# Kernel tuning notes

Hardware: AMD Instinct MI355X
Metric: run time of the kernel (lower is better)

## Reference

```python
import jax, jax.numpy as jnp
import numpy as np

N_QUBITS = 6
DIM = 2 ** N_QUBITS  # 64


def _b(t, nd):
    # broadcast a (B,) per-sample angle factor (or scalar) against a state slice of rank nd
    if jnp.ndim(t) == 0:
        return t
    return t.reshape((t.shape[0],) + (1,) * (nd - 1))


def _ry(state, theta, q):
    ax = q + 1
    s0 = jnp.take(state, 0, axis=ax)
    s1 = jnp.take(state, 1, axis=ax)
    h = theta * 0.5
    c = _b(jnp.cos(h), s0.ndim)
    s = _b(jnp.sin(h), s0.ndim)
    return jnp.stack([c * s0 - s * s1, s * s0 + c * s1], axis=ax)


def _rx(state, theta, q):
    ax = q + 1
    s0 = jnp.take(state, 0, axis=ax)
    s1 = jnp.take(state, 1, axis=ax)
    h = theta * 0.5
    c = _b(jnp.cos(h), s0.ndim)
    s = _b(jnp.sin(h), s0.ndim)
    return jnp.stack([c * s0 - 1j * s * s1, -1j * s * s0 + c * s1], axis=ax)


def _rz(state, theta, q):
    ax = q + 1
    s0 = jnp.take(state, 0, axis=ax)
    s1 = jnp.take(state, 1, axis=ax)
    h = theta * 0.5
    p0 = _b(jnp.exp(-1j * h), s0.ndim)
    p1 = _b(jnp.exp(1j * h), s0.ndim)
    return jnp.stack([p0 * s0, p1 * s1], axis=ax)


def _cnot(state, ctrl, tgt):
    ca = ctrl + 1
    s0 = jnp.take(state, 0, axis=ca)
    s1 = jnp.take(state, 1, axis=ca)
    ta = tgt + 1 if tgt < ctrl else tgt  # target axis after removing control axis
    s1 = jnp.flip(s1, axis=ta)
    return jnp.stack([s0, s1], axis=ca)


def quantum_circuit(inputs, weights):
    # inputs: (B, 6) float; weights: (5, 6) float -> (B, 6) PauliZ expectations
    B = inputs.shape[0]
    scaled = jnp.clip(inputs, -1.0, 1.0) * jnp.pi
    state = jnp.zeros((B,) + (2,) * N_QUBITS, dtype=jnp.complex64)
    state = state.at[(slice(None),) + (0,) * N_QUBITS].set(1.0)
    for i in range(N_QUBITS):
        state = _ry(state, scaled[:, i], i)
    for i in range(N_QUBITS):
        state = _rx(state, weights[0, i], i)
        state = _rz(state, weights[1, i], i)
    for i in range(N_QUBITS - 1):
        state = _cnot(state, i, i + 1)
    state = _cnot(state, N_QUBITS - 1, 0)
    for i in range(N_QUBITS):
        state = _ry(state, weights[2, i], i)
        state = _rz(state, weights[3, i], i)
    for i in range(0, N_QUBITS, 2):
        state = _cnot(state, i, (i + 1) % N_QUBITS)
    for i in range(N_QUBITS):
        state = _rx(state, weights[4, i], i)
    probs = (state.real ** 2 + state.imag ** 2).reshape(B, DIM)
    # Z eigenvalue table: qubit q is bit (5-q) of the flat index
    k = jnp.arange(DIM)
    z = (1 - 2 * ((k[None, :] >> (N_QUBITS - 1 - jnp.arange(N_QUBITS)[:, None])) & 1)).astype(jnp.float32)
    return probs @ z.T  # (B, 6)


def setup_inputs() -> dict:
    key = jax.random.key(0)
    ks = jax.random.split(key, 13)
    B, n_symptoms, n_dep, nq = 262144, 128, 20, N_QUBITS

    def lin(k, fi, fo):
        bound = 1.0 / np.sqrt(fi)
        kw, kb = jax.random.split(k)
        W = jax.random.uniform(kw, (fi, fo), jnp.float32, -bound, bound)
        b = jax.random.uniform(kb, (fo,), jnp.float32, -bound, bound)
        return W, b

    x = jax.random.normal(ks[0], (B, n_symptoms), jnp.float32)
    W1, b1 = lin(ks[1], n_symptoms, 32)
    W2, b2 = lin(ks[2], 32, 16)
    W3, b3 = lin(ks[3], 16, nq)
    qw = jax.random.normal(ks[4], (5, nq), jnp.float32)
    W4, b4 = lin(ks[5], nq, 16)
    W5, b5 = lin(ks[6], 16, n_dep)
    return {"x": x, "W1": W1, "b1": b1, "W2": W2, "b2": b2, "W3": W3, "b3": b3,
            "qw": qw, "W4": W4, "b4": b4, "W5": W5, "b5": b5}


def reference(x, W1, b1, W2, b2, W3, b3, qw, W4, b4, W5, b5):
    h = jax.nn.relu(x @ W1 + b1)            # Dropout(0.2) is identity at eval
    h = jax.nn.relu(h @ W2 + b2)
    pre = jnp.tanh(h @ W3 + b3)             # (B, 6)
    # Original detaches before the quantum circuit -> stop_gradient for fidelity
    q_out = quantum_circuit(jax.lax.stop_gradient(pre), jax.lax.stop_gradient(qw))
    h = jax.nn.relu(q_out @ W4 + b4)
    return h @ W5 + b5                      # (B, n_departments)
```

## Files before the change

kernel.cpp:

```cpp
#include <hip/hip_runtime.h>
#include <hip/hip_bf16.h>
#include <math.h>

#define PI_F 3.14159265358979323846f

typedef float f32x4 __attribute__((ext_vector_type(4)));
typedef short bf16x8 __attribute__((ext_vector_type(8)));

__device__ __forceinline__ unsigned short bf_hi(float f) {
    return (unsigned short)(__float_as_uint(f) >> 16);
}
__device__ __forceinline__ float from_bf(unsigned short h) {
    return __uint_as_float(((unsigned)h) << 16);
}

__global__ __launch_bounds__(64) void build_u(const float* __restrict__ qw,
                                              float* __restrict__ Umat) {
    const int l = threadIdx.x;
    const int b = blockIdx.x;

    float ar = (l == b) ? 1.0f : 0.0f;
    float ai = 0.0f;

    #pragma unroll
    for (int i = 0; i < 6; ++i) {
        const int mask = 1 << (5 - i);
        float th = 0.5f * qw[0 * 6 + i];
        float c = cosf(th), sn = sinf(th);
        float pr = __shfl_xor(ar, mask);
        float pi = __shfl_xor(ai, mask);
        float nr = c * ar + sn * pi;
        float ni = c * ai - sn * pr;
        ar = nr; ai = ni;
        th = 0.5f * qw[1 * 6 + i];
        c = cosf(th); sn = sinf(th);
        float zn = (l & mask) ? 1.0f : -1.0f;
        nr = c * ar - zn * sn * ai;
        ni = c * ai + zn * sn * ar;
        ar = nr; ai = ni;
    }

    #pragma unroll
    for (int i = 0; i < 6; ++i) {
        const int ctrl = i, tgt = (i + 1) % 6;
        const int cm = 1 << (5 - ctrl), tm = 1 << (5 - tgt);
        float pr = __shfl_xor(ar, tm);
        float pi = __shfl_xor(ai, tm);
        bool take = (l & cm) != 0;
        ar = take ? pr : ar;
        ai = take ? pi : ai;
    }

    #pragma unroll
    for (int i = 0; i < 6; ++i) {
        const int mask = 1 << (5 - i);
        float th = 0.5f * qw[2 * 6 + i];
        float c = cosf(th), sn = sinf(th);
        float pr = __shfl_xor(ar, mask);
        float pi = __shfl_xor(ai, mask);
        float sg = (l & mask) ? sn : -sn;
        float nr = c * ar + sg * pr;
        float ni = c * ai + sg * pi;
        ar = nr; ai = ni;
        th = 0.5f * qw[3 * 6 + i];
        c = cosf(th); sn = sinf(th);
        float zn = (l & mask) ? 1.0f : -1.0f;
        nr = c * ar - zn * sn * ai;
        ni = c * ai + zn * sn * ar;
        ar = nr; ai = ni;
    }

    #pragma unroll
    for (int i = 0; i < 6; i += 2) {
        const int cm = 1 << (5 - i), tm = 1 << (5 - (i + 1));
        float pr = __shfl_xor(ar, tm);
        float pi = __shfl_xor(ai, tm);
        bool take = (l & cm) != 0;
        ar = take ? pr : ar;
        ai = take ? pi : ai;
    }

    #pragma unroll
    for (int i = 0; i < 6; ++i) {
        const int mask = 1 << (5 - i);
        float th = 0.5f * qw[4 * 6 + i];
        float c = cosf(th), sn = sinf(th);
        float pr = __shfl_xor(ar, mask);
        float pi = __shfl_xor(ai, mask);
        float nr = c * ar + sn * pi;
        float ni = c * ai - sn * pr;
        ar = nr; ai = ni;
    }

    Umat[(l * 64 + b) * 2 + 0] = ar;
    Umat[(l * 64 + b) * 2 + 1] = ai;
}

__global__ __launch_bounds__(64) void convert_all(
    const float* __restrict__ Umat, const float* __restrict__ W1,
    unsigned short* __restrict__ Ubf, unsigned short* __restrict__ W1bf)
{
    const int l = threadIdx.x;
    bf16x8* out8 = reinterpret_cast<bf16x8*>(Ubf);

    #pragma unroll
    for (int ri = 0; ri < 2; ++ri) {
        #pragma unroll
        for (int t = 0; t < 4; ++t) {
            #pragma unroll
            for (int h = 0; h < 2; ++h) {
                const int vf = (ri * 4 + t) * 2 + h;
                bf16x8 vh, vl;
                #pragma unroll
                for (int e = 0; e < 8; ++e) {
                    const int k = 16 * t + (l & 15);
                    const int j = h * 32 + (l >> 4) * 8 + e;
                    float v = Umat[k * 128 + j * 2 + ri];
                    unsigned short hh = bf_hi(v);
                    vh[e] = (short)hh;
                    vl[e] = (short)bf_hi(v - from_bf(hh));
                }
                out8[(vf * 2 + 0) * 64 + l] = vh;
                out8[(vf * 2 + 1) * 64 + l] = vl;
            }
        }
    }

    bf16x8* w8 = reinterpret_cast<bf16x8*>(W1bf);
    #pragma unroll
    for (int ks = 0; ks < 4; ++ks) {
        #pragma unroll
        for (int nt = 0; nt < 2; ++nt) {
            bf16x8 vh, vl;
            #pragma unroll
            for (int e = 0; e < 8; ++e) {
                float v = W1[(ks * 32 + (l >> 4) * 8 + e) * 32 + nt * 16 + (l & 15)];
                unsigned short hh = bf_hi(v);
                vh[e] = (short)hh;
                vl[e] = (short)bf_hi(v - from_bf(hh));
            }
            w8[((ks * 2 + nt) * 2 + 0) * 64 + l] = vh;
            w8[((ks * 2 + nt) * 2 + 1) * 64 + l] = vl;
        }
    }
}

__device__ __forceinline__ void front_tail(
    const float h1[32],
    const float* __restrict__ W2, const float* __restrict__ b2,
    const float* __restrict__ W3, const float* __restrict__ b3,
    float lo[8], float hi[8])
{
    float h2[16];
    #pragma unroll
    for (int o = 0; o < 16; ++o) h2[o] = b2[o];
    #pragma unroll
    for (int j = 0; j < 32; ++j) {
        #pragma unroll
        for (int o = 0; o < 16; ++o) h2[o] = fmaf(h1[j], W2[j * 16 + o], h2[o]);
    }
    #pragma unroll
    for (int o = 0; o < 16; ++o) h2[o] = fmaxf(h2[o], 0.0f);

    float cq[6], sq[6];
    #pragma unroll
    for (int q = 0; q < 6; ++q) {
        float t = b3[q];
        #pragma unroll
        for (int j = 0; j < 16; ++j) t = fmaf(h2[j], W3[j * 6 + q], t);
        t = tanhf(t);
        t = fminf(1.0f, fmaxf(-1.0f, t));
        float half = t * (0.5f * PI_F);
        sq[q] = sinf(half);
        cq[q] = cosf(half);
    }

    {
        float f3[2] = {cq[3], sq[3]};
        float f4[2] = {cq[4], sq[4]};
        float f5[2] = {cq[5], sq[5]};
        #pragma unroll
        for (int m = 0; m < 8; ++m)
            lo[m] = f3[(m >> 2) & 1] * f4[(m >> 1) & 1] * f5[m & 1];
        float f0[2] = {cq[0], sq[0]};
        float f1[2] = {cq[1], sq[1]};
        float f2[2] = {cq[2], sq[2]};
        #pragma unroll
        for (int m = 0; m < 8; ++m)
            hi[m] = f0[(m >> 2) & 1] * f1[(m >> 1) & 1] * f2[m & 1];
    }
}

__global__ __launch_bounds__(256) void front_mfma(
    const float* __restrict__ x,
    const unsigned short* __restrict__ W1bf, const float* __restrict__ b1,
    const float* __restrict__ W2, const float* __restrict__ b2,
    const float* __restrict__ W3, const float* __restrict__ b3,
    float* __restrict__ tab, int B)
{
    __shared__ float h1lds[256][33];

    const int tid  = threadIdx.x;
    const int wv   = tid >> 6;
    const int lane = tid & 63;
    const int g    = lane >> 4;
    const int c    = lane & 15;
    const long blk = (long)blockIdx.x * 256;

    const bf16x8* Wb = reinterpret_cast<const bf16x8*>(W1bf);

    #pragma unroll
    for (int mt = 0; mt < 4; ++mt) {
        long t0 = blk + wv * 64 + mt * 16 + c;
        const int srow = (int)((t0 < B) ? t0 : (B - 1));
        const float* xrow = x + (size_t)srow * 128;

        f32x4 acc0 = (f32x4)0.0f, acc1 = (f32x4)0.0f;

        #pragma unroll
        for (int ks = 0; ks < 4; ++ks) {
            f32x4 xa = __builtin_nontemporal_load(
                reinterpret_cast<const f32x4*>(xrow + ks * 32 + g * 8));
            f32x4 xb = __builtin_nontemporal_load(
                reinterpret_cast<const f32x4*>(xrow + ks * 32 + g * 8 + 4));
            bf16x8 Ah, Al;
            #pragma unroll
            for (int e = 0; e < 4; ++e) {
                unsigned short hh = bf_hi(xa[e]);
                Ah[e] = (short)hh;
                Al[e] = (short)bf_hi(xa[e] - from_bf(hh));
            }
            #pragma unroll
            for (int e = 0; e < 4; ++e) {
                unsigned short hh = bf_hi(xb[e]);
                Ah[4 + e] = (short)hh;
                Al[4 + e] = (short)bf_hi(xb[e] - from_bf(hh));
            }

            bf16x8 B0h = Wb[((ks * 2 + 0) * 2 + 0) * 64 + lane];
            bf16x8 B0l = Wb[((ks * 2 + 0) * 2 + 1) * 64 + lane];
            bf16x8 B1h = Wb[((ks * 2 + 1) * 2 + 0) * 64 + lane];
            bf16x8 B1l = Wb[((ks * 2 + 1) * 2 + 1) * 64 + lane];

            acc0 = __builtin_amdgcn_mfma_f32_16x16x32_bf16(Ah, B0h, acc0, 0, 0, 0);
            acc0 = __builtin_amdgcn_mfma_f32_16x16x32_bf16(Al, B0h, acc0, 0, 0, 0);
            acc0 = __builtin_amdgcn_mfma_f32_16x16x32_bf16(Ah, B0l, acc0, 0, 0, 0);
            acc1 = __builtin_amdgcn_mfma_f32_16x16x32_bf16(Ah, B1h, acc1, 0, 0, 0);
            acc1 = __builtin_amdgcn_mfma_f32_16x16x32_bf16(Al, B1h, acc1, 0, 0, 0);
            acc1 = __builtin_amdgcn_mfma_f32_16x16x32_bf16(Ah, B1l, acc1, 0, 0, 0);
        }

        #pragma unroll
        for (int r = 0; r < 4; ++r) {
            h1lds[wv * 64 + mt * 16 + g * 4 + r][c]      = acc0[r];
            h1lds[wv * 64 + mt * 16 + g * 4 + r][16 + c] = acc1[r];
        }
    }

    __syncthreads();

    const int s = (int)(blk + tid);
    float h1[32];
    #pragma unroll
    for (int o = 0; o < 32; ++o) h1[o] = fmaxf(h1lds[tid][o] + b1[o], 0.0f);

    float lo[8], hi[8];
    front_tail(h1, W2, b2, W3, b3, lo, hi);

    if (s < B) {
        #pragma unroll
        for (int i = 0; i < 8; ++i)
            __builtin_nontemporal_store(lo[i], &tab[(size_t)i * B + s]);
        #pragma unroll
        for (int i = 0; i < 8; ++i)
            __builtin_nontemporal_store(hi[i], &tab[(size_t)(8 + i) * B + s]);
    }
}

__global__ __launch_bounds__(256) void gemv_mfma(
    const float* __restrict__ tab,
    const unsigned short* __restrict__ Ubf,
    const float* __restrict__ W4, const float* __restrict__ b4,
    const float* __restrict__ W5, const float* __restrict__ b5,
    float* __restrict__ out, int B)
{
    __shared__ float qlds[64][8];

    const int tid  = threadIdx.x;
    const int wv   = tid >> 6;
    const int lane = tid & 63;
    const int g    = lane >> 4;
    const int c    = lane & 15;
    const long blk = (long)blockIdx.x * 64;
    const int s    = (int)(blk + wv * 16 + c);
    const int s_ld = (s < B) ? s : (B - 1);

    float tl[8], th[8];
    #pragma unroll
    for (int i = 0; i < 8; ++i)
        tl[i] = __builtin_nontemporal_load(&tab[(size_t)i * B + s_ld]);
    #pragma unroll
    for (int i = 0; i < 8; ++i)
        th[i] = __builtin_nontemporal_load(&tab[(size_t)(8 + i) * B + s_ld]);

    float bh0 = (g == 0) ? th[0] : (g == 1) ? th[1] : (g == 2) ? th[2] : th[3];
    float bh1 = (g == 0) ? th[4] : (g == 1) ? th[5] : (g == 2) ? th[6] : th[7];

    bf16x8 Ah0, Al0, Ah1, Al1;
    #pragma unroll
    for (int e = 0; e < 8; ++e) {
        float p0 = bh0 * tl[e];
        unsigned short h0 = bf_hi(p0);
        Ah0[e] = (short)h0;
        Al0[e] = (short)bf_hi(p0 - from_bf(h0));
        float p1 = bh1 * tl[e];
        unsigned short h1 = bf_hi(p1);
        Ah1[e] = (short)h1;
        Al1[e] = (short)bf_hi(p1 - from_bf(h1));
    }

    const bf16x8* Ub = reinterpret_cast<const bf16x8*>(Ubf);

    f32x4 accre[4], accim[4];
    #pragma unroll
    for (int t = 0; t < 4; ++t) { accre[t] = (f32x4)0.0f; accim[t] = (f32x4)0.0f; }

    #pragma unroll
    for (int t = 0; t < 4; ++t) {
        bf16x8 B0h = Ub[(((0 * 4 + t) * 2 + 0) * 2 + 0) * 64 + lane];
        bf16x8 B0l = Ub[(((0 * 4 + t) * 2 + 0) * 2 + 1) * 64 + lane];
        bf16x8 B1h = Ub[(((0 * 4 + t) * 2 + 1) * 2 + 0) * 64 + lane];
        bf16x8 B1l = Ub[(((0 * 4 + t) * 2 + 1) * 2 + 1) * 64 + lane];
        accre[t] = __builtin_amdgcn_mfma_f32_16x16x32_bf16(Ah0, B0h, accre[t], 0, 0, 0);
        accre[t] = __builtin_amdgcn_mfma_f32_16x16x32_bf16(Al0, B0h, accre[t], 0, 0, 0);
        accre[t] = __builtin_amdgcn_mfma_f32_16x16x32_bf16(Ah0, B0l, accre[t], 0, 0, 0);
        accre[t] = __builtin_amdgcn_mfma_f32_16x16x32_bf16(Ah1, B1h, accre[t], 0, 0, 0);
        accre[t] = __builtin_amdgcn_mfma_f32_16x16x32_bf16(Al1, B1h, accre[t], 0, 0, 0);
        accre[t] = __builtin_amdgcn_mfma_f32_16x16x32_bf16(Ah1, B1l, accre[t], 0, 0, 0);
    }
    #pragma unroll
    for (int t = 0; t < 4; ++t) {
        bf16x8 B0h = Ub[(((1 * 4 + t) * 2 + 0) * 2 + 0) * 64 + lane];
        bf16x8 B0l = Ub[(((1 * 4 + t) * 2 + 0) * 2 + 1) * 64 + lane];
        bf16x8 B1h = Ub[(((1 * 4 + t) * 2 + 1) * 2 + 0) * 64 + lane];
        bf16x8 B1l = Ub[(((1 * 4 + t) * 2 + 1) * 2 + 1) * 64 + lane];
        accim[t] = __builtin_amdgcn_mfma_f32_16x16x32_bf16(Ah0, B0h, accim[t], 0, 0, 0);
        accim[t] = __builtin_amdgcn_mfma_f32_16x16x32_bf16(Al0, B0h, accim[t], 0, 0, 0);
        accim[t] = __builtin_amdgcn_mfma_f32_16x16x32_bf16(Ah0, B0l, accim[t], 0, 0, 0);
        accim[t] = __builtin_amdgcn_mfma_f32_16x16x32_bf16(Ah1, B1h, accim[t], 0, 0, 0);
        accim[t] = __builtin_amdgcn_mfma_f32_16x16x32_bf16(Al1, B1h, accim[t], 0, 0, 0);
        accim[t] = __builtin_amdgcn_mfma_f32_16x16x32_bf16(Ah1, B1l, accim[t], 0, 0, 0);
    }

    #pragma unroll
    for (int r = 0; r < 4; ++r) {
        float p0 = accre[0][r] * accre[0][r] + accim[0][r] * accim[0][r];
        float p1 = accre[1][r] * accre[1][r] + accim[1][r] * accim[1][r];
        float p2 = accre[2][r] * accre[2][r] + accim[2][r] * accim[2][r];
        float p3 = accre[3][r] * accre[3][r] + accim[3][r] * accim[3][r];

        float P0 = p0 + p1 + p2 + p3;
        float P1 = p0 + p1 - p2 - p3;
        float P2 = p0 - p1 + p2 - p3;

        float v = P0;
        #pragma unroll
        for (int st = 0; st < 4; ++st) {
            const int m = 1 << st;
            float prt = __shfl_xor(v, m);
            v = (lane & m) ? (prt - v) : (prt + v);
        }
        #pragma unroll
        for (int st = 0; st < 4; ++st) P1 += __shfl_xor(P1, 1 << st);
        #pragma unroll
        for (int st = 0; st < 4; ++st) P2 += __shfl_xor(P2, 1 << st);

        const int sl = wv * 16 + g * 4 + r;
        if (c == 0) { qlds[sl][0] = P1; qlds[sl][1] = P2; }
        if (c == 8) qlds[sl][2] = v;
        if (c == 4) qlds[sl][3] = v;
        if (c == 2) qlds[sl][4] = v;
        if (c == 1) qlds[sl][5] = v;
    }

    __syncthreads();

    if (tid < 64) {
        const int so = (int)(blk + tid);
        if (so < B) {
            float qv[6];
            #pragma unroll
            for (int i = 0; i < 6; ++i) qv[i] = qlds[tid][i];

            float h4[16];
            #pragma unroll
            for (int o = 0; o < 16; ++o) h4[o] = b4[o];
            #pragma unroll
            for (int q = 0; q < 6; ++q) {
                #pragma unroll
                for (int o = 0; o < 16; ++o) h4[o] = fmaf(qv[q], W4[q * 16 + o], h4[o]);
            }
            #pragma unroll
            for (int o = 0; o < 16; ++o) h4[o] = fmaxf(h4[o], 0.0f);

            float o5[20];
            #pragma unroll
            for (int o = 0; o < 20; ++o) {
                float t = b5[o];
                #pragma unroll
                for (int j = 0; j < 16; ++j) t = fmaf(h4[j], W5[j * 20 + o], t);
                o5[o] = t;
            }

            f32x4* outv = reinterpret_cast<f32x4*>(out + (size_t)so * 20);
            #pragma unroll
            for (int i = 0; i < 5; ++i) {
                f32x4 v = {o5[4 * i], o5[4 * i + 1], o5[4 * i + 2], o5[4 * i + 3]};
                __builtin_nontemporal_store(v, &outv[i]);
            }
        }
    }
}

extern "C" void kernel_launch(void* const* d_in, const int* in_sizes, int n_in,
                              void* d_out, int out_size, void* d_ws, size_t ws_size,
                              hipStream_t stream) {
    const float* x  = (const float*)d_in[0];
    const float* W1 = (const float*)d_in[1];
    const float* b1 = (const float*)d_in[2];
    const float* W2 = (const float*)d_in[3];
    const float* b2 = (const float*)d_in[4];
    const float* W3 = (const float*)d_in[5];
    const float* b3 = (const float*)d_in[6];
    const float* qw = (const float*)d_in[7];
    const float* W4 = (const float*)d_in[8];
    const float* b4 = (const float*)d_in[9];
    const float* W5 = (const float*)d_in[10];
    const float* b5 = (const float*)d_in[11];
    float* out = (float*)d_out;

    const int B = in_sizes[0] / 128;

    float* Umat = (float*)d_ws;
    unsigned short* Ubf  = (unsigned short*)((float*)d_ws + 8192);
    unsigned short* W1bf = (unsigned short*)((float*)d_ws + 16384);
    float* tab  = (float*)d_ws + 20480;

    build_u<<<64, 64, 0, stream>>>(qw, Umat);
    convert_all<<<1, 64, 0, stream>>>(Umat, W1, Ubf, W1bf);
    front_mfma<<<(B + 255) / 256, 256, 0, stream>>>(
        x, W1bf, b1, W2, b2, W3, b3, tab, B);
    gemv_mfma<<<(B + 63) / 64, 256, 0, stream>>>(
        tab, Ubf, W4, b4, W5, b5, out, B);
}
```

Measured before the change: 101.3 us.

## Fuse front MLP and quantum-unitary GEMV kernels into one, staging via LDS

Merges the front MLP kernel and the unitary-GEMV/back-MLP kernel into a single kernel. The per-sample product-state factors go through shared memory instead of a global scratch table, and each block now handles 256 samples by looping over four 16-row tiles per wave. This removes one launch and the global write and read of the intermediate table. In exchange the fused kernel holds more live state and more shared memory, which may lower occupancy, and the GEMV loop is no longer unrolled.

```diff
diff --git a/kernel.cpp b/kernel.cpp
--- a/kernel.cpp
+++ b/kernel.cpp
@@ -191,14 +191,17 @@
     }
 }
 
-__global__ __launch_bounds__(256) void front_mfma(
+__global__ __launch_bounds__(256) void fused_all(
     const float* __restrict__ x,
     const unsigned short* __restrict__ W1bf, const float* __restrict__ b1,
     const float* __restrict__ W2, const float* __restrict__ b2,
     const float* __restrict__ W3, const float* __restrict__ b3,
-    float* __restrict__ tab, int B)
+    const unsigned short* __restrict__ Ubf,
+    const float* __restrict__ W4, const float* __restrict__ b4,
+    const float* __restrict__ W5, const float* __restrict__ b5,
+    float* __restrict__ out, int B)
 {
-    __shared__ float h1lds[256][33];
+    __shared__ float smem[256 * 33];
 
     const int tid  = threadIdx.x;
     const int wv   = tid >> 6;
@@ -207,212 +210,203 @@
     const int c    = lane & 15;
     const long blk = (long)blockIdx.x * 256;
 
-    const bf16x8* Wb = reinterpret_cast<const bf16x8*>(W1bf);
-
-    #pragma unroll
-    for (int mt = 0; mt < 4; ++mt) {
-        long t0 = blk + wv * 64 + mt * 16 + c;
-        const int srow = (int)((t0 < B) ? t0 : (B - 1));
-        const float* xrow = x + (size_t)srow * 128;
-
-        f32x4 acc0 = (f32x4)0.0f, acc1 = (f32x4)0.0f;
-
-        #pragma unroll
-        for (int ks = 0; ks < 4; ++ks) {
-            f32x4 xa = __builtin_nontemporal_load(
-                reinterpret_cast<const f32x4*>(xrow + ks * 32 + g * 8));
-            f32x4 xb = __builtin_nontemporal_load(
-                reinterpret_cast<const f32x4*>(xrow + ks * 32 + g * 8 + 4));
-            bf16x8 Ah, Al;
-            #pragma unroll
-            for (int e = 0; e < 4; ++e) {
-                unsigned short hh = bf_hi(xa[e]);
-                Ah[e] = (short)hh;
-                Al[e] = (short)bf_hi(xa[e] - from_bf(hh));
-            }
-            #pragma unroll
-            for (int e = 0; e < 4; ++e) {
-                unsigned short hh = bf_hi(xb[e]);
-                Ah[4 + e] = (short)hh;
-                Al[4 + e] = (short)bf_hi(xb[e] - from_bf(hh));
-            }
-
-            bf16x8 B0h = Wb[((ks * 2 + 0) * 2 + 0) * 64 + lane];
-            bf16x8 B0l = Wb[((ks * 2 + 0) * 2 + 1) * 64 + lane];
-            bf16x8 B1h = Wb[((ks * 2 + 1) * 2 + 0) * 64 + lane];
-            bf16x8 B1l = Wb[((ks * 2 + 1) * 2 + 1) * 64 + lane];
-
-            acc0 = __builtin_amdgcn_mfma_f32_16x16x32_bf16(Ah, B0h, acc0, 0, 0, 0);
-            acc0 = __builtin_amdgcn_mfma_f32_16x16x32_bf16(Al, B0h, acc0, 0, 0, 0);
-            acc0 = __builtin_amdgcn_mfma_f32_16x16x32_bf16(Ah, B0l, acc0, 0, 0, 0);
-            acc1 = __builtin_amdgcn_mfma_f32_16x16x32_bf16(Ah, B1h, acc1, 0, 0, 0);
-            acc1 = __builtin_amdgcn_mfma_f32_16x16x32_bf16(Al, B1h, acc1, 0, 0, 0);
-            acc1 = __builtin_amdgcn_mfma_f32_16x16x32_bf16(Ah, B1l, acc1, 0, 0, 0);
-        }
-
-        #pragma unroll
-        for (int r = 0; r < 4; ++r) {
-            h1lds[wv * 64 + mt * 16 + g * 4 + r][c]      = acc0[r];
-            h1lds[wv * 64 + mt * 16 + g * 4 + r][16 + c] = acc1[r];
+    {
+        const bf16x8* Wb = reinterpret_cast<const bf16x8*>(W1bf);
+
+        #pragma unroll
+        for (int mt = 0; mt < 4; ++mt) {
+            long t0 = blk + wv * 64 + mt * 16 + c;
+            const int srow = (int)((t0 < B) ? t0 : (B - 1));
+            const float* xrow = x + (size_t)srow * 128;
+
+            f32x4 acc0 = (f32x4)0.0f, acc1 = (f32x4)0.0f;
+
+            #pragma unroll
+            for (int ks = 0; ks < 4; ++ks) {
+                f32x4 xa = __builtin_nontemporal_load(
+                    reinterpret_cast<const f32x4*>(xrow + ks * 32 + g * 8));
+                f32x4 xb = __builtin_nontemporal_load(
+                    reinterpret_cast<const f32x4*>(xrow + ks * 32 + g * 8 + 4));
+                bf16x8 Ah, Al;
+                #pragma unroll
+                for (int e = 0; e < 4; ++e) {
+                    unsigned short hh = bf_hi(xa[e]);
+                    Ah[e] = (short)hh;
+                    Al[e] = (short)bf_hi(xa[e] - from_bf(hh));
+                }
+                #pragma unroll
+                for (int e = 0; e < 4; ++e) {
+                    unsigned short hh = bf_hi(xb[e]);
+                    Ah[4 + e] = (short)hh;
+                    Al[4 + e] = (short)bf_hi(xb[e] - from_bf(hh));
+                }
+
+                bf16x8 B0h = Wb[((ks * 2 + 0) * 2 + 0) * 64 + lane];
+                bf16x8 B0l = Wb[((ks * 2 + 0) * 2 + 1) * 64 + lane];
+                bf16x8 B1h = Wb[((ks * 2 + 1) * 2 + 0) * 64 + lane];
+                bf16x8 B1l = Wb[((ks * 2 + 1) * 2 + 1) * 64 + lane];
+
+                acc0 = __builtin_amdgcn_mfma_f32_16x16x32_bf16(Ah, B0h, acc0, 0, 0, 0);
+                acc0 = __builtin_amdgcn_mfma_f32_16x16x32_bf16(Al, B0h, acc0, 0, 0, 0);
+                acc0 = __builtin_amdgcn_mfma_f32_16x16x32_bf16(Ah, B0l, acc0, 0, 0, 0);
+                acc1 = __builtin_amdgcn_mfma_f32_16x16x32_bf16(Ah, B1h, acc1, 0, 0, 0);
+                acc1 = __builtin_amdgcn_mfma_f32_16x16x32_bf16(Al, B1h, acc1, 0, 0, 0);
+                acc1 = __builtin_amdgcn_mfma_f32_16x16x32_bf16(Ah, B1l, acc1, 0, 0, 0);
+            }
+
+            #pragma unroll
+            for (int r = 0; r < 4; ++r) {
+                smem[(wv * 64 + mt * 16 + g * 4 + r) * 33 + c]      = acc0[r];
+                smem[(wv * 64 + mt * 16 + g * 4 + r) * 33 + 16 + c] = acc1[r];
+            }
         }
     }
 
     __syncthreads();
 
-    const int s = (int)(blk + tid);
-    float h1[32];
-    #pragma unroll
-    for (int o = 0; o < 32; ++o) h1[o] = fmaxf(h1lds[tid][o] + b1[o], 0.0f);
-
-    float lo[8], hi[8];
-    front_tail(h1, W2, b2, W3, b3, lo, hi);
-
-    if (s < B) {
-        #pragma unroll
-        for (int i = 0; i < 8; ++i)
-            __builtin_nontemporal_store(lo[i], &tab[(size_t)i * B + s]);
-        #pragma unroll
-        for (int i = 0; i < 8; ++i)
-            __builtin_nontemporal_store(hi[i], &tab[(size_t)(8 + i) * B + s]);
-    }
-}
-
-__global__ __launch_bounds__(256) void gemv_mfma(
-    const float* __restrict__ tab,
-    const unsigned short* __restrict__ Ubf,
-    const float* __restrict__ W4, const float* __restrict__ b4,
-    const float* __restrict__ W5, const float* __restrict__ b5,
-    float* __restrict__ out, int B)
-{
-    __shared__ float qlds[64][8];
-
-    const int tid  = threadIdx.x;
-    const int wv   = tid >> 6;
-    const int lane = tid & 63;
-    const int g    = lane >> 4;
-    const int c    = lane & 15;
-    const long blk = (long)blockIdx.x * 64;
-    const int s    = (int)(blk + wv * 16 + c);
-    const int s_ld = (s < B) ? s : (B - 1);
-
-    float tl[8], th[8];
-    #pragma unroll
-    for (int i = 0; i < 8; ++i)
-        tl[i] = __builtin_nontemporal_load(&tab[(size_t)i * B + s_ld]);
-    #pragma unroll
-    for (int i = 0; i < 8; ++i)
-        th[i] = __builtin_nontemporal_load(&tab[(size_t)(8 + i) * B + s_ld]);
-
-    float bh0 = (g == 0) ? th[0] : (g == 1) ? th[1] : (g == 2) ? th[2] : th[3];
-    float bh1 = (g == 0) ? th[4] : (g == 1) ? th[5] : (g == 2) ? th[6] : th[7];
-
-    bf16x8 Ah0, Al0, Ah1, Al1;
-    #pragma unroll
-    for (int e = 0; e < 8; ++e) {
-        float p0 = bh0 * tl[e];
-        unsigned short h0 = bf_hi(p0);
-        Ah0[e] = (short)h0;
-        Al0[e] = (short)bf_hi(p0 - from_bf(h0));
-        float p1 = bh1 * tl[e];
-        unsigned short h1 = bf_hi(p1);
-        Ah1[e] = (short)h1;
-        Al1[e] = (short)bf_hi(p1 - from_bf(h1));
-    }
-
-    const bf16x8* Ub = reinterpret_cast<const bf16x8*>(Ubf);
-
-    f32x4 accre[4], accim[4];
-    #pragma unroll
-    for (int t = 0; t < 4; ++t) { accre[t] = (f32x4)0.0f; accim[t] = (f32x4)0.0f; }
-
-    #pragma unroll
-    for (int t = 0; t < 4; ++t) {
-        bf16x8 B0h = Ub[(((0 * 4 + t) * 2 + 0) * 2 + 0) * 64 + lane];
-        bf16x8 B0l = Ub[(((0 * 4 + t) * 2 + 0) * 2 + 1) * 64 + lane];
-        bf16x8 B1h = Ub[(((0 * 4 + t) * 2 + 1) * 2 + 0) * 64 + lane];
-        bf16x8 B1l = Ub[(((0 * 4 + t) * 2 + 1) * 2 + 1) * 64 + lane];
-        accre[t] = __builtin_amdgcn_mfma_f32_16x16x32_bf16(Ah0, B0h, accre[t], 0, 0, 0);
-        accre[t] = __builtin_amdgcn_mfma_f32_16x16x32_bf16(Al0, B0h, accre[t], 0, 0, 0);
-        accre[t] = __builtin_amdgcn_mfma_f32_16x16x32_bf16(Ah0, B0l, accre[t], 0, 0, 0);
-        accre[t] = __builtin_amdgcn_mfma_f32_16x16x32_bf16(Ah1, B1h, accre[t], 0, 0, 0);
-        accre[t] = __builtin_amdgcn_mfma_f32_16x16x32_bf16(Al1, B1h, accre[t], 0, 0, 0);
-        accre[t] = __builtin_amdgcn_mfma_f32_16x16x32_bf16(Ah1, B1l, accre[t], 0, 0, 0);
-    }
-    #pragma unroll
-    for (int t = 0; t < 4; ++t) {
-        bf16x8 B0h = Ub[(((1 * 4 + t) * 2 + 0) * 2 + 0) * 64 + lane];
-        bf16x8 B0l = Ub[(((1 * 4 + t) * 2 + 0) * 2 + 1) * 64 + lane];
-        bf16x8 B1h = Ub[(((1 * 4 + t) * 2 + 1) * 2 + 0) * 64 + lane];
-        bf16x8 B1l = Ub[(((1 * 4 + t) * 2 + 1) * 2 + 1) * 64 + lane];
-        accim[t] = __builtin_amdgcn_mfma_f32_16x16x32_bf16(Ah0, B0h, accim[t], 0, 0, 0);
-        accim[t] = __builtin_amdgcn_mfma_f32_16x16x32_bf16(Al0, B0h, accim[t], 0, 0, 0);
-        accim[t] = __builtin_amdgcn_mfma_f32_16x16x32_bf16(Ah0, B0l, accim[t], 0, 0, 0);
-        accim[t] = __builtin_amdgcn_mfma_f32_16x16x32_bf16(Ah1, B1h, accim[t], 0, 0, 0);
-        accim[t] = __builtin_amdgcn_mfma_f32_16x16x32_bf16(Al1, B1h, accim[t], 0, 0, 0);
-        accim[t] = __builtin_amdgcn_mfma_f32_16x16x32_bf16(Ah1, B1l, accim[t], 0, 0, 0);
-    }
-
-    #pragma unroll
-    for (int r = 0; r < 4; ++r) {
-        float p0 = accre[0][r] * accre[0][r] + accim[0][r] * accim[0][r];
-        float p1 = accre[1][r] * accre[1][r] + accim[1][r] * accim[1][r];
-        float p2 = accre[2][r] * accre[2][r] + accim[2][r] * accim[2][r];
-        float p3 = accre[3][r] * accre[3][r] + accim[3][r] * accim[3][r];
-
-        float P0 = p0 + p1 + p2 + p3;
-        float P1 = p0 + p1 - p2 - p3;
-        float P2 = p0 - p1 + p2 - p3;
-
-        float v = P0;
-        #pragma unroll
-        for (int st = 0; st < 4; ++st) {
-            const int m = 1 << st;
-            float prt = __shfl_xor(v, m);
-            v = (lane & m) ? (prt - v) : (prt + v);
-        }
-        #pragma unroll
-        for (int st = 0; st < 4; ++st) P1 += __shfl_xor(P1, 1 << st);
-        #pragma unroll
-        for (int st = 0; st < 4; ++st) P2 += __shfl_xor(P2, 1 << st);
-
-        const int sl = wv * 16 + g * 4 + r;
-        if (c == 0) { qlds[sl][0] = P1; qlds[sl][1] = P2; }
-        if (c == 8) qlds[sl][2] = v;
-        if (c == 4) qlds[sl][3] = v;
-        if (c == 2) qlds[sl][4] = v;
-        if (c == 1) qlds[sl][5] = v;
+    {
+        float h1[32];
+        #pragma unroll
+        for (int o = 0; o < 32; ++o) h1[o] = fmaxf(smem[tid * 33 + o] + b1[o], 0.0f);
+
+        float lo[8], hi[8];
+        front_tail(h1, W2, b2, W3, b3, lo, hi);
+
+        __syncthreads();
+
+        #pragma unroll
+        for (int i = 0; i < 8; ++i) smem[tid * 17 + i]     = lo[i];
+        #pragma unroll
+        for (int i = 0; i < 8; ++i) smem[tid * 17 + 8 + i] = hi[i];
     }
 
     __syncthreads();
 
-    if (tid < 64) {
-        const int so = (int)(blk + tid);
-        if (so < B) {
-            float qv[6];
-            #pragma unroll
-            for (int i = 0; i < 6; ++i) qv[i] = qlds[tid][i];
-
-            float h4[16];
-            #pragma unroll
-            for (int o = 0; o < 16; ++o) h4[o] = b4[o];
-            #pragma unroll
-            for (int q = 0; q < 6; ++q) {
-                #pragma unroll
-                for (int o = 0; o < 16; ++o) h4[o] = fmaf(qv[q], W4[q * 16 + o], h4[o]);
-            }
-            #pragma unroll
-            for (int o = 0; o < 16; ++o) h4[o] = fmaxf(h4[o], 0.0f);
-
-            float o5[20];
-            #pragma unroll
-            for (int o = 0; o < 20; ++o) {
-                float t = b5[o];
-                #pragma unroll
-                for (int j = 0; j < 16; ++j) t = fmaf(h4[j], W5[j * 20 + o], t);
-                o5[o] = t;
-            }
-
-            f32x4* outv = reinterpret_cast<f32x4*>(out + (size_t)so * 20);
+    {
+        const bf16x8* Ub = reinterpret_cast<const bf16x8*>(Ubf);
+
+        #pragma unroll 1
+        for (int mt = 0; mt < 4; ++mt) {
+            const int sl = wv * 64 + mt * 16 + c;
+
+            float tl[8], th[8];
+            #pragma unroll
+            for (int i = 0; i < 8; ++i) tl[i] = smem[sl * 17 + i];
+            #pragma unroll
+            for (int i = 0; i < 8; ++i) th[i] = smem[sl * 17 + 8 + i];
+
+            float bh0 = (g == 0) ? th[0] : (g == 1) ? th[1] : (g == 2) ? th[2] : th[3];
+            float bh1 = (g == 0) ? th[4] : (g == 1) ? th[5] : (g == 2) ? th[6] : th[7];
+
+            bf16x8 Ah0, Al0, Ah1, Al1;
+            #pragma unroll
+            for (int e = 0; e < 8; ++e) {
+                float p0 = bh0 * tl[e];
+                unsigned short h0 = bf_hi(p0);
+                Ah0[e] = (short)h0;
+                Al0[e] = (short)bf_hi(p0 - from_bf(h0));
+                float p1 = bh1 * tl[e];
+                unsigned short h1 = bf_hi(p1);
+                Ah1[e] = (short)h1;
+                Al1[e] = (short)bf_hi(p1 - from_bf(h1));
+            }
+
+            f32x4 accre[4], accim[4];
+            #pragma unroll
+            for (int t = 0; t < 4; ++t) { accre[t] = (f32x4)0.0f; accim[t] = (f32x4)0.0f; }
+
+            #pragma unroll
+            for (int t = 0; t < 4; ++t) {
+                bf16x8 B0h = Ub[(((0 * 4 + t) * 2 + 0) * 2 + 0) * 64 + lane];
+                bf16x8 B0l = Ub[(((0 * 4 + t) * 2 + 0) * 2 + 1) * 64 + lane];
+                bf16x8 B1h = Ub[(((0 * 4 + t) * 2 + 1) * 2 + 0) * 64 + lane];
+                bf16x8 B1l = Ub[(((0 * 4 + t) * 2 + 1) * 2 + 1) * 64 + lane];
+                accre[t] = __builtin_amdgcn_mfma_f32_16x16x32_bf16(Ah0, B0h, accre[t], 0, 0, 0);
+                accre[t] = __builtin_amdgcn_mfma_f32_16x16x32_bf16(Al0, B0h, accre[t], 0, 0, 0);
+                accre[t] = __builtin_amdgcn_mfma_f32_16x16x32_bf16(Ah0, B0l, accre[t], 0, 0, 0);
+                accre[t] = __builtin_amdgcn_mfma_f32_16x16x32_bf16(Ah1, B1h, accre[t], 0, 0, 0);
+                accre[t] = __builtin_amdgcn_mfma_f32_16x16x32_bf16(Al1, B1h, accre[t], 0, 0, 0);
+                accre[t] = __builtin_amdgcn_mfma_f32_16x16x32_bf16(Ah1, B1l, accre[t], 0, 0, 0);
+            }
+            #pragma unroll
+            for (int t = 0; t < 4; ++t) {
+                bf16x8 B0h = Ub[(((1 * 4 + t) * 2 + 0) * 2 + 0) * 64 + lane];
+                bf16x8 B0l = Ub[(((1 * 4 + t) * 2 + 0) * 2 + 1) * 64 + lane];
+                bf16x8 B1h = Ub[(((1 * 4 + t) * 2 + 1) * 2 + 0) * 64 + lane];
+                bf16x8 B1l = Ub[(((1 * 4 + t) * 2 + 1) * 2 + 1) * 64 + lane];
+                accim[t] = __builtin_amdgcn_mfma_f32_16x16x32_bf16(Ah0, B0h, accim[t], 0, 0, 0);
+                accim[t] = __builtin_amdgcn_mfma_f32_16x16x32_bf16(Al0, B0h, accim[t], 0, 0, 0);
+                accim[t] = __builtin_amdgcn_mfma_f32_16x16x32_bf16(Ah0, B0l, accim[t], 0, 0, 0);
+                accim[t] = __builtin_amdgcn_mfma_f32_16x16x32_bf16(Ah1, B1h, accim[t], 0, 0, 0);
+                accim[t] = __builtin_amdgcn_mfma_f32_16x16x32_bf16(Al1, B1h, accim[t], 0, 0, 0);
+                accim[t] = __builtin_amdgcn_mfma_f32_16x16x32_bf16(Ah1, B1l, accim[t], 0, 0, 0);
+            }
+
+            #pragma unroll
+            for (int r = 0; r < 4; ++r) {
+                float p0 = accre[0][r] * accre[0][r] + accim[0][r] * accim[0][r];
+                float p1 = accre[1][r] * accre[1][r] + accim[1][r] * accim[1][r];
+                float p2 = accre[2][r] * accre[2][r] + accim[2][r] * accim[2][r];
+                float p3 = accre[3][r] * accre[3][r] + accim[3][r] * accim[3][r];
+
+                float P0 = p0 + p1 + p2 + p3;
+                float P1 = p0 + p1 - p2 - p3;
+                float P2 = p0 - p1 + p2 - p3;
+
+                float v = P0;
+                #pragma unroll
+                for (int st = 0; st < 4; ++st) {
+                    const int m = 1 << st;
+                    float prt = __shfl_xor(v, m);
+                    v = (lane & m) ? (prt - v) : (prt + v);
+                }
+                #pragma unroll
+                for (int st = 0; st < 4; ++st) P1 += __shfl_xor(P1, 1 << st);
+                #pragma unroll
+                for (int st = 0; st < 4; ++st) P2 += __shfl_xor(P2, 1 << st);
+
+                const int so = wv * 64 + mt * 16 + g * 4 + r;
+                float* qrow = &smem[256 * 17 + so * 8];
+                if (c == 0) { qrow[0] = P1; qrow[1] = P2; }
+                if (c == 8) qrow[2] = v;
+                if (c == 4) qrow[3] = v;
+                if (c == 2) qrow[4] = v;
+                if (c == 1) qrow[5] = v;
+            }
+        }
+    }
+
+    __syncthreads();
+
+    {
+        const int s = (int)(blk + tid);
+        const float* qrow = &smem[256 * 17 + tid * 8];
+        float qv[6];
+        #pragma unroll
+        for (int i = 0; i < 6; ++i) qv[i] = qrow[i];
+
+        float h4[16];
+        #pragma unroll
+        for (int o = 0; o < 16; ++o) h4[o] = b4[o];
+        #pragma unroll
+        for (int q = 0; q < 6; ++q) {
+            #pragma unroll
+            for (int o = 0; o < 16; ++o) h4[o] = fmaf(qv[q], W4[q * 16 + o], h4[o]);
+        }
+        #pragma unroll
+        for (int o = 0; o < 16; ++o) h4[o] = fmaxf(h4[o], 0.0f);
+
+        float o5[20];
+        #pragma unroll
+        for (int o = 0; o < 20; ++o) {
+            float t = b5[o];
+            #pragma unroll
+            for (int j = 0; j < 16; ++j) t = fmaf(h4[j], W5[j * 20 + o], t);
+            o5[o] = t;
+        }
+
+        if (s < B) {
+            f32x4* outv = reinterpret_cast<f32x4*>(out + (size_t)s * 20);
             #pragma unroll
             for (int i = 0; i < 5; ++i) {
                 f32x4 v = {o5[4 * i], o5[4 * i + 1], o5[4 * i + 2], o5[4 * i + 3]};
@@ -444,12 +438,9 @@
     float* Umat = (float*)d_ws;
     unsigned short* Ubf  = (unsigned short*)((float*)d_ws + 8192);
     unsigned short* W1bf = (unsigned short*)((float*)d_ws + 16384);
-    float* tab  = (float*)d_ws + 20480;
 
     build_u<<<64, 64, 0, stream>>>(qw, Umat);
     convert_all<<<1, 64, 0, stream>>>(Umat, W1, Ubf, W1bf);
-    front_mfma<<<(B + 255) / 256, 256, 0, stream>>>(
-        x, W1bf, b1, W2, b2, W3, b3, tab, B);
-    gemv_mfma<<<(B + 63) / 64, 256, 0, stream>>>(
-        tab, Ubf, W4, b4, W5, b5, out, B);
-}
+    fused_all<<<(B + 255) / 256, 256, 0, stream>>>(
+        x, W1bf, b1, W2, b2, W3, b3, Ubf, W4, b4, W5, b5, out, B);
+}
```

Result: slower. 110.9 us (+9.4%).

## Stage x tiles through LDS with coalesced loads in front_mfma

Applied to the files above, without the earlier changes.

Instead of each lane loading its own strided 32-byte slices of x rows directly for the MFMA A-operand, the block now loads 32-column K-slices of 256 rows cooperatively with fully coalesced 16-byte loads into padded shared memory, then reads MFMA fragments from LDS. The loop order is inverted (ks outer, mt inner) so W1 fragments are loaded once per K-step, and accumulators for all four M-tiles are kept live. This adds two block barriers per K-step, more accumulator registers and an LDS round trip, in exchange for better global-memory coalescing.

```diff
diff --git a/kernel.cpp b/kernel.cpp
--- a/kernel.cpp
+++ b/kernel.cpp
@@ -198,7 +198,7 @@
     const float* __restrict__ W3, const float* __restrict__ b3,
     float* __restrict__ tab, int B)
 {
-    __shared__ float h1lds[256][33];
+    __shared__ float smem[256 * 36];
 
     const int tid  = threadIdx.x;
     const int wv   = tid >> 6;
@@ -207,22 +207,38 @@
     const int c    = lane & 15;
     const long blk = (long)blockIdx.x * 256;
 
+    const f32x4* xg = reinterpret_cast<const f32x4*>(x);
     const bf16x8* Wb = reinterpret_cast<const bf16x8*>(W1bf);
 
-    #pragma unroll
-    for (int mt = 0; mt < 4; ++mt) {
-        long t0 = blk + wv * 64 + mt * 16 + c;
-        const int srow = (int)((t0 < B) ? t0 : (B - 1));
-        const float* xrow = x + (size_t)srow * 128;
-
-        f32x4 acc0 = (f32x4)0.0f, acc1 = (f32x4)0.0f;
-
-        #pragma unroll
-        for (int ks = 0; ks < 4; ++ks) {
-            f32x4 xa = __builtin_nontemporal_load(
-                reinterpret_cast<const f32x4*>(xrow + ks * 32 + g * 8));
-            f32x4 xb = __builtin_nontemporal_load(
-                reinterpret_cast<const f32x4*>(xrow + ks * 32 + g * 8 + 4));
+    f32x4 acc0[4], acc1[4];
+    #pragma unroll
+    for (int mt = 0; mt < 4; ++mt) { acc0[mt] = (f32x4)0.0f; acc1[mt] = (f32x4)0.0f; }
+
+    #pragma unroll 1
+    for (int ks = 0; ks < 4; ++ks) {
+        #pragma unroll
+        for (int i = 0; i < 8; ++i) {
+            const int flat = i * 256 + tid;
+            const int row = flat >> 3;
+            const int c4  = flat & 7;
+            long srow = blk + row;
+            if (srow >= B) srow = B - 1;
+            f32x4 v = __builtin_nontemporal_load(&xg[(size_t)srow * 32 + ks * 8 + c4]);
+            *reinterpret_cast<f32x4*>(&smem[row * 36 + c4 * 4]) = v;
+        }
+        __syncthreads();
+
+        bf16x8 B0h = Wb[((ks * 2 + 0) * 2 + 0) * 64 + lane];
+        bf16x8 B0l = Wb[((ks * 2 + 0) * 2 + 1) * 64 + lane];
+        bf16x8 B1h = Wb[((ks * 2 + 1) * 2 + 0) * 64 + lane];
+        bf16x8 B1l = Wb[((ks * 2 + 1) * 2 + 1) * 64 + lane];
+
+        #pragma unroll
+        for (int mt = 0; mt < 4; ++mt) {
+            const int row = wv * 64 + mt * 16 + c;
+            f32x4 xa = *reinterpret_cast<const f32x4*>(&smem[row * 36 + g * 8]);
+            f32x4 xb = *reinterpret_cast<const f32x4*>(&smem[row * 36 + g * 8 + 4]);
+
             bf16x8 Ah, Al;
             #pragma unroll
             for (int e = 0; e < 4; ++e) {
@@ -237,23 +253,22 @@
                 Al[4 + e] = (short)bf_hi(xb[e] - from_bf(hh));
             }
 
-            bf16x8 B0h = Wb[((ks * 2 + 0) * 2 + 0) * 64 + lane];
-            bf16x8 B0l = Wb[((ks * 2 + 0) * 2 + 1) * 64 + lane];
-            bf16x8 B1h = Wb[((ks * 2 + 1) * 2 + 0) * 64 + lane];
-            bf16x8 B1l = Wb[((ks * 2 + 1) * 2 + 1) * 64 + lane];
-
-            acc0 = __builtin_amdgcn_mfma_f32_16x16x32_bf16(Ah, B0h, acc0, 0, 0, 0);
-            acc0 = __builtin_amdgcn_mfma_f32_16x16x32_bf16(Al, B0h, acc0, 0, 0, 0);
-            acc0 = __builtin_amdgcn_mfma_f32_16x16x32_bf16(Ah, B0l, acc0, 0, 0, 0);
-            acc1 = __builtin_amdgcn_mfma_f32_16x16x32_bf16(Ah, B1h, acc1, 0, 0, 0);
-            acc1 = __builtin_amdgcn_mfma_f32_16x16x32_bf16(Al, B1h, acc1, 0, 0, 0);
-            acc1 = __builtin_amdgcn_mfma_f32_16x16x32_bf16(Ah, B1l, acc1, 0, 0, 0);
-        }
-
+            acc0[mt] = __builtin_amdgcn_mfma_f32_16x16x32_bf16(Ah, B0h, acc0[mt], 0, 0, 0);
+            acc0[mt] = __builtin_amdgcn_mfma_f32_16x16x32_bf16(Al, B0h, acc0[mt], 0, 0, 0);
+            acc0[mt] = __builtin_amdgcn_mfma_f32_16x16x32_bf16(Ah, B0l, acc0[mt], 0, 0, 0);
+            acc1[mt] = __builtin_amdgcn_mfma_f32_16x16x32_bf16(Ah, B1h, acc1[mt], 0, 0, 0);
+            acc1[mt] = __builtin_amdgcn_mfma_f32_16x16x32_bf16(Al, B1h, acc1[mt], 0, 0, 0);
+            acc1[mt] = __builtin_amdgcn_mfma_f32_16x16x32_bf16(Ah, B1l, acc1[mt], 0, 0, 0);
+        }
+        __syncthreads();
+    }
+
+    #pragma unroll
+    for (int mt = 0; mt < 4; ++mt) {
         #pragma unroll
         for (int r = 0; r < 4; ++r) {
-            h1lds[wv * 64 + mt * 16 + g * 4 + r][c]      = acc0[r];
-            h1lds[wv * 64 + mt * 16 + g * 4 + r][16 + c] = acc1[r];
+            smem[(wv * 64 + mt * 16 + g * 4 + r) * 33 + c]      = acc0[mt][r];
+            smem[(wv * 64 + mt * 16 + g * 4 + r) * 33 + 16 + c] = acc1[mt][r];
         }
     }
 
@@ -262,7 +277,7 @@
     const int s = (int)(blk + tid);
     float h1[32];
     #pragma unroll
-    for (int o = 0; o < 32; ++o) h1[o] = fmaxf(h1lds[tid][o] + b1[o], 0.0f);
+    for (int o = 0; o < 32; ++o) h1[o] = fmaxf(smem[tid * 33 + o] + b1[o], 0.0f);
 
     float lo[8], hi[8];
     front_tail(h1, W2, b2, W3, b3, lo, hi);
```

Measured after the change: 97.46 us (median of 2 runs). -3.8%, faster.
